# Optimization experiments

Hardware: AMD Instinct MI355X
Metric: run time of the kernel (lower is better)

## Reference

```python
import jax, jax.numpy as jnp
import numpy as np

SEQ_LEN, BATCH, INPUT_SIZE, HIDDEN_SIZE = 2048, 512, 64, 128


def setup_inputs() -> dict:
    key = jax.random.key(0)
    kx, kwh, kbh, kwi, kbi = jax.random.split(key, 5)
    s_h = 1.0 / np.sqrt(HIDDEN_SIZE)
    s_i = 1.0 / np.sqrt(INPUT_SIZE)
    return {
        "x": jax.random.normal(kx, (SEQ_LEN, BATCH, INPUT_SIZE), dtype=jnp.float32),
        "Wh": jax.random.normal(kwh, (HIDDEN_SIZE, HIDDEN_SIZE), dtype=jnp.float32) * s_h,
        "bh": jax.random.normal(kbh, (HIDDEN_SIZE,), dtype=jnp.float32) * s_h,
        "Wi": jax.random.normal(kwi, (HIDDEN_SIZE, INPUT_SIZE), dtype=jnp.float32) * s_i,
        "bi": jax.random.normal(kbi, (HIDDEN_SIZE,), dtype=jnp.float32) * s_i,
    }


def reference(x, Wh, bh, Wi, bi):
    # Elman RNN: h_t = tanh(h_{t-1} @ Wh^T + bh + x_t @ Wi^T + bi)
    # Precompute the input projection for all timesteps in one big GEMM,
    # then scan the (inherently sequential) hidden recurrence.
    x_proj = jnp.einsum('sbi,hi->sbh', x, Wi) + bi + bh  # (S, B, H)

    h0 = jnp.zeros((x.shape[1], Wh.shape[0]), dtype=x.dtype)

    def step(h_prev, xp_t):
        h = jnp.tanh(h_prev @ Wh.T + xp_t)
        return h, h

    h_last, h_seq = jax.lax.scan(step, h0, x_proj)
    # match torch module: (h_seq [S,B,H], final hidden [B,H])
    return h_seq, h_last
```

## Files before the change

### kernel.cpp

```cpp
#include <hip/hip_runtime.h>
#include <hip/hip_bf16.h>

#define SEQ   2048
#define BATCH 512
#define ISZ   64
#define HSZ   128

__launch_bounds__(256, 2)
__global__ void rnn_fused(const float* __restrict__ x,
                          const float* __restrict__ Wh,
                          const float* __restrict__ bh,
                          const float* __restrict__ Wi,
                          const float* __restrict__ bi,
                          float* __restrict__ out)
{
    __shared__ __align__(16) float xbuf[2][32][ISZ];
    __shared__ __align__(16) float hbuf[2][HSZ];

    const int tid  = threadIdx.x;
    const int b    = blockIdx.x;
    const int h    = tid >> 1;
    const int half = tid & 1;

    float whr[64];
    {
        const float4* wp = (const float4*)(Wh + h * HSZ + half * 64);
        #pragma unroll
        for (int j = 0; j < 16; ++j) {
            float4 v = wp[j];
            whr[4*j+0] = v.x; whr[4*j+1] = v.y; whr[4*j+2] = v.z; whr[4*j+3] = v.w;
        }
    }
    float wir[32];
    {
        const float4* wp = (const float4*)(Wi + h * ISZ + half * 32);
        #pragma unroll
        for (int j = 0; j < 8; ++j) {
            float4 v = wp[j];
            wir[4*j+0] = v.x; wir[4*j+1] = v.y; wir[4*j+2] = v.z; wir[4*j+3] = v.w;
        }
    }
    const float bias = bh[h] + bi[h];

    if (tid < HSZ) hbuf[0][tid] = 0.f;
    const int s  = tid >> 4;
    const int i4 = tid & 15;
    {
        float4 c0 = *(const float4*)(x + ((0  + s) * BATCH + b) * ISZ + i4 * 4);
        float4 c1 = *(const float4*)(x + ((16 + s) * BATCH + b) * ISZ + i4 * 4);
        *(float4*)&xbuf[0][s][i4 * 4]      = c0;
        *(float4*)&xbuf[0][16 + s][i4 * 4] = c1;
    }
    __syncthreads();

    float4 p0 = make_float4(0.f, 0.f, 0.f, 0.f);
    float4 p1 = p0;
    float  hn = 0.f;

    #pragma unroll 2
    for (int t = 0; t < SEQ; ++t) {
        const int cb  = (t >> 5) & 1;
        const int cur = t & 1;
        const int nxt = cur ^ 1;

        if ((t & 31) == 0 && t + 32 < SEQ) {
            p0 = *(const float4*)(x + ((t + 32 + s) * BATCH + b) * ISZ + i4 * 4);
            p1 = *(const float4*)(x + ((t + 48 + s) * BATCH + b) * ISZ + i4 * 4);
        }
        if ((t & 31) == 16 && t + 16 < SEQ) {
            *(float4*)&xbuf[cb ^ 1][s][i4 * 4]      = p0;
            *(float4*)&xbuf[cb ^ 1][16 + s][i4 * 4] = p1;
        }

        float a0 = 0.f, a1 = 0.f, a2 = 0.f, a3 = 0.f;
        const float4* hb = (const float4*)(&hbuf[cur][half * 64]);
        #pragma unroll
        for (int j = 0; j < 16; ++j) {
            float4 hv = hb[j];
            a0 += whr[4*j+0] * hv.x; a1 += whr[4*j+1] * hv.y;
            a2 += whr[4*j+2] * hv.z; a3 += whr[4*j+3] * hv.w;
        }
        const float4* xb = (const float4*)(&xbuf[cb][t & 31][half * 32]);
        #pragma unroll
        for (int j = 0; j < 8; ++j) {
            float4 xv = xb[j];
            a0 += wir[4*j+0] * xv.x; a1 += wir[4*j+1] * xv.y;
            a2 += wir[4*j+2] * xv.z; a3 += wir[4*j+3] * xv.w;
        }
        float acc = (a0 + a1) + (a2 + a3);
        acc += __shfl_xor(acc, 1, 64);
        acc += bias;

        float e = __expf(2.f * acc);
        hn = 1.f - 2.f * __builtin_amdgcn_rcpf(e + 1.f);

        if (half == 0) {
            hbuf[nxt][h] = hn;
            out[(size_t)(t * BATCH + b) * HSZ + h] = hn;
        }

        asm volatile("s_waitcnt lgkmcnt(0)\n\ts_barrier" ::: "memory");
    }

    if (half == 0) {
        out[(size_t)SEQ * BATCH * HSZ + b * HSZ + h] = hn;
    }
}

extern "C" void kernel_launch(void* const* d_in, const int* in_sizes, int n_in,
                              void* d_out, int out_size, void* d_ws, size_t ws_size,
                              hipStream_t stream)
{
    const float* x  = (const float*)d_in[0];
    const float* Wh = (const float*)d_in[1];
    const float* bh = (const float*)d_in[2];
    const float* Wi = (const float*)d_in[3];
    const float* bi = (const float*)d_in[4];
    float* out = (float*)d_out;

    dim3 grid(BATCH);
    dim3 block(256);
    hipLaunchKernelGGL(rnn_fused, grid, block, 0, stream, x, Wh, bh, Wi, bi, out);
}
```

Baseline: 1.969 ms.

## Shrink RNN block to 128 threads with 4-output register tiles and DPP reductions

Each block now uses 128 threads, each computing partial dot products for 4 output rows over a quarter of the reduction dimension. Partials are reduced across 4 lanes with DPP quad permutes instead of a shuffle. The hidden-state buffer is padded per k-group to avoid LDS bank conflicts. The aim is to reuse each LDS-loaded h/x value across 4 outputs, cutting LDS traffic and barrier cost per step. In exchange, register pressure rises to about 192 weight floats per thread, and each wave has fewer threads to hide latency.

```diff
diff --git a/kernel.cpp b/kernel.cpp
--- a/kernel.cpp
+++ b/kernel.cpp
@@ -1,12 +1,20 @@
 #include <hip/hip_runtime.h>
-#include <hip/hip_bf16.h>
 
 #define SEQ   2048
 #define BATCH 512
 #define ISZ   64
 #define HSZ   128
 
-__launch_bounds__(256, 2)
+#define HPAD 36
+#define HTOT (4*HPAD)
+
+template<int CTRL>
+__device__ __forceinline__ float qadd(float v) {
+    int p = __builtin_amdgcn_update_dpp(0, __float_as_int(v), CTRL, 0xF, 0xF, true);
+    return v + __int_as_float(p);
+}
+
+__launch_bounds__(128, 1)
 __global__ void rnn_fused(const float* __restrict__ x,
                           const float* __restrict__ Wh,
                           const float* __restrict__ bh,
@@ -15,47 +23,54 @@
                           float* __restrict__ out)
 {
     __shared__ __align__(16) float xbuf[2][32][ISZ];
-    __shared__ __align__(16) float hbuf[2][HSZ];
+    __shared__ __align__(16) float hbuf[2][HTOT];
 
-    const int tid  = threadIdx.x;
-    const int b    = blockIdx.x;
-    const int h    = tid >> 1;
-    const int half = tid & 1;
+    const int tid = threadIdx.x;
+    const int b   = blockIdx.x;
+    const int og  = tid >> 2;
+    const int kg  = tid & 3;
 
-    float whr[64];
-    {
-        const float4* wp = (const float4*)(Wh + h * HSZ + half * 64);
-        #pragma unroll
-        for (int j = 0; j < 16; ++j) {
-            float4 v = wp[j];
-            whr[4*j+0] = v.x; whr[4*j+1] = v.y; whr[4*j+2] = v.z; whr[4*j+3] = v.w;
-        }
-    }
-    float wir[32];
-    {
-        const float4* wp = (const float4*)(Wi + h * ISZ + half * 32);
+    float whr[4][32];
+    float wir[4][16];
+    #pragma unroll
+    for (int i = 0; i < 4; ++i) {
+        const int o = og + 32*i;
+        const float4* wp = (const float4*)(Wh + o*HSZ + kg*32);
         #pragma unroll
         for (int j = 0; j < 8; ++j) {
             float4 v = wp[j];
-            wir[4*j+0] = v.x; wir[4*j+1] = v.y; wir[4*j+2] = v.z; wir[4*j+3] = v.w;
+            whr[i][4*j+0]=v.x; whr[i][4*j+1]=v.y; whr[i][4*j+2]=v.z; whr[i][4*j+3]=v.w;
+        }
+        const float4* ip = (const float4*)(Wi + o*ISZ + kg*16);
+        #pragma unroll
+        for (int j = 0; j < 4; ++j) {
+            float4 v = ip[j];
+            wir[i][4*j+0]=v.x; wir[i][4*j+1]=v.y; wir[i][4*j+2]=v.z; wir[i][4*j+3]=v.w;
         }
     }
-    const float bias = bh[h] + bi[h];
+    const int   oown = og + 32*kg;
+    const float bsel = bh[oown] + bi[oown];
 
-    if (tid < HSZ) hbuf[0][tid] = 0.f;
-    const int s  = tid >> 4;
-    const int i4 = tid & 15;
+    for (int k = tid; k < 2*HTOT; k += 128) ((float*)hbuf)[k] = 0.f;
+
+    const int s = tid >> 3;
+    const int c = tid & 7;
     {
-        float4 c0 = *(const float4*)(x + ((0  + s) * BATCH + b) * ISZ + i4 * 4);
-        float4 c1 = *(const float4*)(x + ((16 + s) * BATCH + b) * ISZ + i4 * 4);
-        *(float4*)&xbuf[0][s][i4 * 4]      = c0;
-        *(float4*)&xbuf[0][16 + s][i4 * 4] = c1;
+        const float* xr0 = x + ((size_t)(0  + s)*BATCH + b)*ISZ;
+        const float* xr1 = x + ((size_t)(16 + s)*BATCH + b)*ISZ;
+        float4 a0 = *(const float4*)(xr0 + c*4);
+        float4 a1 = *(const float4*)(xr0 + (c+8)*4);
+        float4 a2 = *(const float4*)(xr1 + c*4);
+        float4 a3 = *(const float4*)(xr1 + (c+8)*4);
+        *(float4*)&xbuf[0][s][c*4]        = a0;
+        *(float4*)&xbuf[0][s][(c+8)*4]    = a1;
+        *(float4*)&xbuf[0][16+s][c*4]     = a2;
+        *(float4*)&xbuf[0][16+s][(c+8)*4] = a3;
     }
     __syncthreads();
 
-    float4 p0 = make_float4(0.f, 0.f, 0.f, 0.f);
-    float4 p1 = p0;
-    float  hn = 0.f;
+    float4 p0 = make_float4(0.f,0.f,0.f,0.f), p1 = p0, p2 = p0, p3 = p0;
+    float  hsel = 0.f;
 
     #pragma unroll 2
     for (int t = 0; t < SEQ; ++t) {
@@ -64,47 +79,70 @@
         const int nxt = cur ^ 1;
 
         if ((t & 31) == 0 && t + 32 < SEQ) {
-            p0 = *(const float4*)(x + ((t + 32 + s) * BATCH + b) * ISZ + i4 * 4);
-            p1 = *(const float4*)(x + ((t + 48 + s) * BATCH + b) * ISZ + i4 * 4);
+            const float* q0 = x + ((size_t)(t+32+s)*BATCH + b)*ISZ;
+            const float* q1 = x + ((size_t)(t+48+s)*BATCH + b)*ISZ;
+            p0 = *(const float4*)(q0 + c*4);
+            p1 = *(const float4*)(q0 + (c+8)*4);
+            p2 = *(const float4*)(q1 + c*4);
+            p3 = *(const float4*)(q1 + (c+8)*4);
         }
         if ((t & 31) == 16 && t + 16 < SEQ) {
-            *(float4*)&xbuf[cb ^ 1][s][i4 * 4]      = p0;
-            *(float4*)&xbuf[cb ^ 1][16 + s][i4 * 4] = p1;
+            const int nb = cb ^ 1;
+            *(float4*)&xbuf[nb][s][c*4]        = p0;
+            *(float4*)&xbuf[nb][s][(c+8)*4]    = p1;
+            *(float4*)&xbuf[nb][16+s][c*4]     = p2;
+            *(float4*)&xbuf[nb][16+s][(c+8)*4] = p3;
         }
 
-        float a0 = 0.f, a1 = 0.f, a2 = 0.f, a3 = 0.f;
-        const float4* hb = (const float4*)(&hbuf[cur][half * 64]);
+        float a0[4], a1[4], a2[4], a3[4];
         #pragma unroll
-        for (int j = 0; j < 16; ++j) {
-            float4 hv = hb[j];
-            a0 += whr[4*j+0] * hv.x; a1 += whr[4*j+1] * hv.y;
-            a2 += whr[4*j+2] * hv.z; a3 += whr[4*j+3] * hv.w;
-        }
-        const float4* xb = (const float4*)(&xbuf[cb][t & 31][half * 32]);
+        for (int i = 0; i < 4; ++i) { a0[i]=0.f; a1[i]=0.f; a2[i]=0.f; a3[i]=0.f; }
+
+        const float4* hb = (const float4*)(&hbuf[cur][kg*HPAD]);
         #pragma unroll
         for (int j = 0; j < 8; ++j) {
-            float4 xv = xb[j];
-            a0 += wir[4*j+0] * xv.x; a1 += wir[4*j+1] * xv.y;
-            a2 += wir[4*j+2] * xv.z; a3 += wir[4*j+3] * xv.w;
+            float4 hv = hb[j];
+            #pragma unroll
+            for (int i = 0; i < 4; ++i) {
+                a0[i] += whr[i][4*j+0]*hv.x; a1[i] += whr[i][4*j+1]*hv.y;
+                a2[i] += whr[i][4*j+2]*hv.z; a3[i] += whr[i][4*j+3]*hv.w;
+            }
         }
-        float acc = (a0 + a1) + (a2 + a3);
-        acc += __shfl_xor(acc, 1, 64);
-        acc += bias;
+        const float4* xv4 = (const float4*)(&xbuf[cb][t & 31][kg*16]);
+        #pragma unroll
+        for (int j = 0; j < 4; ++j) {
+            float4 xv = xv4[j];
+            #pragma unroll
+            for (int i = 0; i < 4; ++i) {
+                a0[i] += wir[i][4*j+0]*xv.x; a1[i] += wir[i][4*j+1]*xv.y;
+                a2[i] += wir[i][4*j+2]*xv.z; a3[i] += wir[i][4*j+3]*xv.w;
+            }
+        }
+
+        float d0 = (a0[0]+a1[0]) + (a2[0]+a3[0]);
+        float d1 = (a0[1]+a1[1]) + (a2[1]+a3[1]);
+        float d2 = (a0[2]+a1[2]) + (a2[2]+a3[2]);
+        float d3 = (a0[3]+a1[3]) + (a2[3]+a3[3]);
+
+        d0 = qadd<0x4E>(qadd<0xB1>(d0));
+        d1 = qadd<0x4E>(qadd<0xB1>(d1));
+        d2 = qadd<0x4E>(qadd<0xB1>(d2));
+        d3 = qadd<0x4E>(qadd<0xB1>(d3));
+
+        float v0  = (kg & 2) ? d2 : d0;
+        float v1  = (kg & 2) ? d3 : d1;
+        float acc = ((kg & 1) ? v1 : v0) + bsel;
 
         float e = __expf(2.f * acc);
-        hn = 1.f - 2.f * __builtin_amdgcn_rcpf(e + 1.f);
+        hsel = 1.f - 2.f * __builtin_amdgcn_rcpf(e + 1.f);
 
-        if (half == 0) {
-            hbuf[nxt][h] = hn;
-            out[(size_t)(t * BATCH + b) * HSZ + h] = hn;
-        }
+        hbuf[nxt][kg*HPAD + og] = hsel;
+        out[((size_t)t*BATCH + b)*HSZ + oown] = hsel;
 
         asm volatile("s_waitcnt lgkmcnt(0)\n\ts_barrier" ::: "memory");
     }
 
-    if (half == 0) {
-        out[(size_t)SEQ * BATCH * HSZ + b * HSZ + h] = hn;
-    }
+    out[(size_t)SEQ*BATCH*HSZ + (size_t)b*HSZ + oown] = hsel;
 }
 
 extern "C" void kernel_launch(void* const* d_in, const int* in_sizes, int n_in,
@@ -119,6 +157,6 @@
     float* out = (float*)d_out;
 
     dim3 grid(BATCH);
-    dim3 block(256);
+    dim3 block(128);
     hipLaunchKernelGGL(rnn_fused, grid, block, 0, stream, x, Wh, bh, Wi, bi, out);
 }
```

New measurement: 1.842 ms. 6.5% less time.
